# Kernel optimization log

Measured on AMD Instinct MI355X. Metric: run time of the kernel, lower is better.

## Reference

```python
import jax, jax.numpy as jnp
import numpy as np

N_QUBITS = 12
N_LAYERS = 3


def _apply_1q(state, U, q):
    # state: (2,)*N_QUBITS complex64, U: (2,2) single-qubit gate on wire q
    r = jnp.tensordot(U, state, axes=([1], [q]))
    return jnp.moveaxis(r, 0, q)


def _apply_cnot(state, c, t):
    M = jnp.array([[1, 0, 0, 0], [0, 1, 0, 0], [0, 0, 0, 1], [0, 0, 1, 0]],
                  jnp.complex64).reshape(2, 2, 2, 2)
    r = jnp.tensordot(M, state, axes=([2, 3], [c, t]))
    return jnp.moveaxis(r, (0, 1), (c, t))


def circuit_expvals(weights):
    # weights: (N_LAYERS, N_QUBITS, 3). Circuit starts from |0...0> (the
    # TorchLayer 'inputs' arg is a dummy and unused in the original qnode).
    state = jnp.zeros((2,) * N_QUBITS, jnp.complex64).at[(0,) * N_QUBITS].set(1.0)
    zero = jnp.zeros((), jnp.complex64)
    for l in range(N_LAYERS):
        for q in range(N_QUBITS):
            tx, ty, tz = weights[l, q, 0], weights[l, q, 1], weights[l, q, 2]
            cx = jnp.cos(tx / 2).astype(jnp.complex64)
            sx = jnp.sin(tx / 2).astype(jnp.complex64)
            RX = jnp.stack([jnp.stack([cx, -1j * sx]), jnp.stack([-1j * sx, cx])])
            cy = jnp.cos(ty / 2).astype(jnp.complex64)
            sy = jnp.sin(ty / 2).astype(jnp.complex64)
            RY = jnp.stack([jnp.stack([cy, -sy]), jnp.stack([sy, cy])])
            tzc = tz.astype(jnp.complex64)
            em, ep = jnp.exp(-1j * tzc / 2), jnp.exp(1j * tzc / 2)
            RZ = jnp.stack([jnp.stack([em, zero]), jnp.stack([zero, ep])])
            # RX then RY then RZ applied to the state => matrix RZ @ RY @ RX
            state = _apply_1q(state, RZ @ RY @ RX, q)
        for q in range(N_QUBITS):
            state = _apply_cnot(state, q, (q + 1) % N_QUBITS)
    probs = state.real ** 2 + state.imag ** 2
    exps = []
    for q in range(N_QUBITS):
        marg = probs.sum(axis=tuple(a for a in range(N_QUBITS) if a != q))  # (2,)
        exps.append(marg[0] - marg[1])  # <Z_q>
    return jnp.stack(exps).astype(jnp.float32)  # (12,)


def setup_inputs() -> dict:
    key = jax.random.key(0)
    ks = jax.random.split(key, 5)
    B = 1048576
    images = jax.random.uniform(ks[0], (B, 1, 4, 4), dtype=jnp.float32)
    qweights = jax.random.normal(ks[1], (N_LAYERS, N_QUBITS, 3), dtype=jnp.float32)
    W1 = jax.random.normal(ks[2], (32, 12), dtype=jnp.float32) * (1.0 / np.sqrt(12))
    b1 = jnp.zeros((32,), jnp.float32)
    W2 = jax.random.normal(ks[3], (16, 32), dtype=jnp.float32) * (1.0 / np.sqrt(32))
    b2 = jnp.zeros((16,), jnp.float32)
    return {"images": images, "qweights": qweights, "W1": W1, "b1": b1,
            "W2": W2, "b2": b2}


def reference(images, qweights, W1, b1, W2, b2):
    # The original forward ignores the amplitude-encoded image state and runs
    # the identical circuit (dummy zero input) for every batch element, so the
    # per-sample result is constant across the batch.
    z = circuit_expvals(qweights)                     # (12,)
    h = jax.nn.relu(z @ W1.T + b1)                    # (32,)
    pix = jax.nn.sigmoid(h @ W2.T + b2)               # (16,)
    B = images.shape[0]
    return jnp.broadcast_to(pix.reshape(1, 1, 4, 4), (B, 1, 4, 4))
```

## Files before the change

kernel.cpp:

```cpp
#include <hip/hip_runtime.h>
#include <math.h>

#define NQ  12
#define NST 4096

__device__ __forceinline__ int P(int i) { return i ^ ((i >> 4) & 0xF); }

__device__ __forceinline__ void apply2(const float4& u0, const float4& u1,
                                       float2& v0, float2& v1) {
    const float n0r = u0.x*v0.x - u0.y*v0.y + u0.z*v1.x - u0.w*v1.y;
    const float n0i = u0.x*v0.y + u0.y*v0.x + u0.z*v1.y + u0.w*v1.x;
    const float n1r = u1.x*v0.x - u1.y*v0.y + u1.z*v1.x - u1.w*v1.y;
    const float n1i = u1.x*v0.y + u1.y*v0.x + u1.z*v1.y + u1.w*v1.x;
    v0 = make_float2(n0r, n0i);
    v1 = make_float2(n1r, n1i);
}

__global__ __launch_bounds__(1024) void circuit_kernel(
    const float* __restrict__ qw,
    const float* __restrict__ W1,
    const float* __restrict__ b1,
    const float* __restrict__ W2,
    const float* __restrict__ b2,
    float* __restrict__ pix)
{
    __shared__ float2 amp[NST];
    __shared__ float2 cs[108];
    __shared__ float4 gmat[36][2];
    __shared__ float  szv[NQ];
    __shared__ float  sh[32];

    const int tid = threadIdx.x;

    for (int i = tid; i < NST; i += 1024) amp[i] = make_float2(0.f, 0.f);
    if (tid == 0) amp[0] = make_float2(1.f, 0.f);
    if (tid < 108) {
        const float a = 0.5f * qw[tid];
        cs[tid] = make_float2(cosf(a), sinf(a));
    }
    __syncthreads();
    if (tid < 36) {
        const float cx = cs[3*tid+0].x, sx = cs[3*tid+0].y;
        const float cy = cs[3*tid+1].x, sy = cs[3*tid+1].y;
        const float cz = cs[3*tid+2].x, sz = cs[3*tid+2].y;
        const float a00r =  cy*cx, a00i =  sy*sx;
        const float a01r = -sy*cx, a01i = -cy*sx;
        const float a10r =  sy*cx, a10i = -cy*sx;
        const float a11r =  cy*cx, a11i = -sy*sx;
        gmat[tid][0] = make_float4(cz*a00r + sz*a00i, cz*a00i - sz*a00r,
                                   cz*a01r + sz*a01i, cz*a01i - sz*a01r);
        gmat[tid][1] = make_float4(cz*a10r - sz*a10i, cz*a10i + sz*a10r,
                                   cz*a11r - sz*a11i, cz*a11i + sz*a11r);
    }
    __syncthreads();

    for (int l = 0; l < 3; ++l) {
        for (int j = 0; j < 6; ++j) {
            const int g = l*12 + 2*j;
            const float4 ua0 = gmat[g][0],   ua1 = gmat[g][1];
            const float4 ub0 = gmat[g+1][0], ub1 = gmat[g+1][1];
            const int pb = 10 - 2*j;
            const int bb = 1 << pb, ba = bb << 1;
            const int base = ((tid >> pb) << (pb + 2)) | (tid & (bb - 1));
            const int i00 = P(base),      i01 = P(base | bb);
            const int i10 = P(base | ba), i11 = P(base | ba | bb);
            float2 v00 = amp[i00], v01 = amp[i01];
            float2 v10 = amp[i10], v11 = amp[i11];
            apply2(ua0, ua1, v00, v10);
            apply2(ua0, ua1, v01, v11);
            apply2(ub0, ub1, v00, v01);
            apply2(ub0, ub1, v10, v11);
            amp[i00] = v00; amp[i01] = v01; amp[i10] = v10; amp[i11] = v11;
            __syncthreads();
        }
        {
            int dst[4]; float2 val[4];
            #pragma unroll
            for (int k = 0; k < 4; ++k) {
                const int f = tid + 1024*k;
                val[k] = amp[P(f)];
                int t = f;
                t ^= t >> 1; t ^= t >> 2; t ^= t >> 4; t ^= t >> 8;
                const int gd = (t & 0x7FF) | (((t ^ (f >> 11)) & 1) << 11);
                dst[k] = P(gd);
            }
            __syncthreads();
            #pragma unroll
            for (int k = 0; k < 4; ++k) amp[dst[k]] = val[k];
            __syncthreads();
        }
    }

    const int lane = tid & 63;
    const int w    = tid >> 6;
    if (w < NQ) {
        const int bit = 1 << (11 - w);
        float s = 0.f;
        for (int i = lane; i < NST; i += 64) {
            const float2 a = amp[P(i)];
            const float pr = a.x*a.x + a.y*a.y;
            s += (i & bit) ? -pr : pr;
        }
        #pragma unroll
        for (int off = 32; off > 0; off >>= 1) s += __shfl_down(s, off, 64);
        if (lane == 0) szv[w] = s;
    }
    __syncthreads();

    if (tid < 32) {
        float acc = b1[tid];
        #pragma unroll
        for (int k = 0; k < 12; ++k) acc += W1[tid*12 + k] * szv[k];
        sh[tid] = acc > 0.f ? acc : 0.f;
    }
    __syncthreads();
    if (tid < 16) {
        float acc = b2[tid];
        #pragma unroll
        for (int k = 0; k < 32; ++k) acc += W2[tid*32 + k] * sh[k];
        pix[tid] = 1.f / (1.f + expf(-acc));
    }
}

__global__ __launch_bounds__(256) void bcast_kernel(
    const float4* __restrict__ pix4, float4* __restrict__ out4)
{
    const int i = blockIdx.x * 256 + threadIdx.x;
    out4[i] = pix4[i & 3];
}

extern "C" void kernel_launch(void* const* d_in, const int* in_sizes, int n_in,
                              void* d_out, int out_size, void* d_ws, size_t ws_size,
                              hipStream_t stream) {
    const float* qw = (const float*)d_in[1];
    const float* W1 = (const float*)d_in[2];
    const float* b1 = (const float*)d_in[3];
    const float* W2 = (const float*)d_in[4];
    const float* b2 = (const float*)d_in[5];
    float* pix = (float*)d_ws;

    circuit_kernel<<<1, 1024, 0, stream>>>(qw, W1, b1, W2, b2, pix);

    const int n4 = out_size / 4;
    bcast_kernel<<<n4 / 256, 256, 0, stream>>>((const float4*)pix,
                                               (float4*)d_out);
}
```

Baseline: 133.4 us.

## Restructure circuit simulation with product-state first layer and 3-qubit register passes

Rewrites the single-block circuit kernel. The first layer is built analytically as a product state, since it acts on |0…0>. The remaining two layers apply three qubits' gates per pass on 8 amplitudes held in registers, with a new swizzle, which cuts the number of barriers and LDS round trips. The CNOT permutation is folded into the store of the last pass of each layer, and the Z expectation values are accumulated in registers during the final pass and then reduced with shuffles. The block size drops to 512 threads. The total runtime is likely dominated by the broadcast kernel writing 16M floats, so the gain is probably small.

```diff
diff --git a/kernel.cpp b/kernel.cpp
--- a/kernel.cpp
+++ b/kernel.cpp
@@ -1,12 +1,20 @@
 #include <hip/hip_runtime.h>
 #include <math.h>
 
-#define NQ  12
-#define NST 4096
-
-__device__ __forceinline__ int P(int i) { return i ^ ((i >> 4) & 0xF); }
-
-__device__ __forceinline__ void apply2(const float4& u0, const float4& u1,
+#define NTH 512
+
+__device__ __forceinline__ int Sw(int i) { return i ^ ((i >> 6) & 7); }
+
+__device__ __forceinline__ int Fr(int i) {
+    int x = i; x ^= x >> 1; x ^= x >> 2; x ^= x >> 4; x ^= x >> 8;
+    return (x & 0x7FF) | (((x ^ (i >> 11)) & 1) << 11);
+}
+
+__device__ __forceinline__ float2 cmul(float2 a, float2 b) {
+    return make_float2(a.x*b.x - a.y*b.y, a.x*b.y + a.y*b.x);
+}
+
+__device__ __forceinline__ void apply2(const float4 u0, const float4 u1,
                                        float2& v0, float2& v1) {
     const float n0r = u0.x*v0.x - u0.y*v0.y + u0.z*v1.x - u0.w*v1.y;
     const float n0i = u0.x*v0.y + u0.y*v0.x + u0.z*v1.y + u0.w*v1.x;
@@ -16,7 +24,51 @@
     v1 = make_float2(n1r, n1i);
 }
 
-__global__ __launch_bounds__(1024) void circuit_kernel(
+template<int PLOW, int MODE>
+__device__ __forceinline__ void do_pass(float2* amp, const float4 (*gmat)[2],
+                                        int gbase, int t, float* zacc) {
+    int base;
+    if      (PLOW == 9) base = t;
+    else if (PLOW == 6) base = ((t >> 6) << 9) | (t & 63);
+    else if (PLOW == 3) base = ((t >> 3) << 6) | (t & 7);
+    else                base = t << 3;
+
+    float2 v[8]; int idx[8];
+    #pragma unroll
+    for (int r = 0; r < 8; ++r) {
+        idx[r] = Sw(base | (r << PLOW));
+        v[r] = amp[idx[r]];
+    }
+    #pragma unroll
+    for (int k = 2; k >= 0; --k) {
+        const int q = 11 - (PLOW + k);
+        const float4 u0 = gmat[gbase + q][0];
+        const float4 u1 = gmat[gbase + q][1];
+        const int m = 1 << k;
+        #pragma unroll
+        for (int r = 0; r < 8; ++r)
+            if (!(r & m)) apply2(u0, u1, v[r], v[r | m]);
+    }
+    if (MODE == 0) {
+        #pragma unroll
+        for (int r = 0; r < 8; ++r) amp[idx[r]] = v[r];
+    } else if (MODE == 1) {
+        __syncthreads();
+        #pragma unroll
+        for (int r = 0; r < 8; ++r) amp[Sw(Fr(base | (r << PLOW)))] = v[r];
+    } else {
+        #pragma unroll
+        for (int r = 0; r < 8; ++r) {
+            const int x = Fr(base | (r << PLOW));
+            const float p = v[r].x*v[r].x + v[r].y*v[r].y;
+            #pragma unroll
+            for (int q = 0; q < 12; ++q)
+                zacc[q] += ((x >> (11 - q)) & 1) ? -p : p;
+        }
+    }
+}
+
+__global__ __launch_bounds__(NTH) void circuit_kernel(
     const float* __restrict__ qw,
     const float* __restrict__ W1,
     const float* __restrict__ b1,
@@ -24,25 +76,19 @@
     const float* __restrict__ b2,
     float* __restrict__ pix)
 {
-    __shared__ float2 amp[NST];
-    __shared__ float2 cs[108];
+    __shared__ float2 amp[4096];
     __shared__ float4 gmat[36][2];
-    __shared__ float  szv[NQ];
+    __shared__ float  zp2[96];
+    __shared__ float  szv[12];
     __shared__ float  sh[32];
 
     const int tid = threadIdx.x;
 
-    for (int i = tid; i < NST; i += 1024) amp[i] = make_float2(0.f, 0.f);
-    if (tid == 0) amp[0] = make_float2(1.f, 0.f);
-    if (tid < 108) {
-        const float a = 0.5f * qw[tid];
-        cs[tid] = make_float2(cosf(a), sinf(a));
-    }
-    __syncthreads();
     if (tid < 36) {
-        const float cx = cs[3*tid+0].x, sx = cs[3*tid+0].y;
-        const float cy = cs[3*tid+1].x, sy = cs[3*tid+1].y;
-        const float cz = cs[3*tid+2].x, sz = cs[3*tid+2].y;
+        float sx, cx, sy, cy, sz, cz;
+        sincosf(0.5f * qw[tid*3+0], &sx, &cx);
+        sincosf(0.5f * qw[tid*3+1], &sy, &cy);
+        sincosf(0.5f * qw[tid*3+2], &sz, &cz);
         const float a00r =  cy*cx, a00i =  sy*sx;
         const float a01r = -sy*cx, a01i = -cy*sx;
         const float a10r =  sy*cx, a10i = -cy*sx;
@@ -54,56 +100,75 @@
     }
     __syncthreads();
 
-    for (int l = 0; l < 3; ++l) {
-        for (int j = 0; j < 6; ++j) {
-            const int g = l*12 + 2*j;
-            const float4 ua0 = gmat[g][0],   ua1 = gmat[g][1];
-            const float4 ub0 = gmat[g+1][0], ub1 = gmat[g+1][1];
-            const int pb = 10 - 2*j;
-            const int bb = 1 << pb, ba = bb << 1;
-            const int base = ((tid >> pb) << (pb + 2)) | (tid & (bb - 1));
-            const int i00 = P(base),      i01 = P(base | bb);
-            const int i10 = P(base | ba), i11 = P(base | ba | bb);
-            float2 v00 = amp[i00], v01 = amp[i01];
-            float2 v10 = amp[i10], v11 = amp[i11];
-            apply2(ua0, ua1, v00, v10);
-            apply2(ua0, ua1, v01, v11);
-            apply2(ub0, ub1, v00, v01);
-            apply2(ub0, ub1, v10, v11);
-            amp[i00] = v00; amp[i01] = v01; amp[i10] = v10; amp[i11] = v11;
-            __syncthreads();
-        }
-        {
-            int dst[4]; float2 val[4];
-            #pragma unroll
-            for (int k = 0; k < 4; ++k) {
-                const int f = tid + 1024*k;
-                val[k] = amp[P(f)];
-                int t = f;
-                t ^= t >> 1; t ^= t >> 2; t ^= t >> 4; t ^= t >> 8;
-                const int gd = (t & 0x7FF) | (((t ^ (f >> 11)) & 1) << 11);
-                dst[k] = P(gd);
-            }
-            __syncthreads();
-            #pragma unroll
-            for (int k = 0; k < 4; ++k) amp[dst[k]] = val[k];
-            __syncthreads();
-        }
-    }
+    {
+        float2 pp = make_float2(1.f, 0.f);
+        #pragma unroll
+        for (int b = 11; b >= 3; --b) {
+            const int q = 11 - b;
+            const float4 g = gmat[q][(tid >> (b - 3)) & 1];
+            pp = cmul(pp, make_float2(g.x, g.y));
+        }
+        float2 c9[2], c10[2], c11[2];
+        #pragma unroll
+        for (int s = 0; s < 2; ++s) {
+            c9[s]  = make_float2(gmat[9][s].x,  gmat[9][s].y);
+            c10[s] = make_float2(gmat[10][s].x, gmat[10][s].y);
+            c11[s] = make_float2(gmat[11][s].x, gmat[11][s].y);
+        }
+        #pragma unroll
+        for (int r = 0; r < 8; ++r) {
+            const float2 v = cmul(pp,
+                cmul(c9[(r>>2)&1], cmul(c10[(r>>1)&1], c11[r&1])));
+            amp[Sw(Fr((tid << 3) | r))] = v;
+        }
+    }
+    __syncthreads();
+
+    float zacc[12];
+    #pragma unroll
+    for (int q = 0; q < 12; ++q) zacc[q] = 0.f;
+
+    do_pass<9,0>(amp, gmat, 12, tid, zacc); __syncthreads();
+    do_pass<6,0>(amp, gmat, 12, tid, zacc); __syncthreads();
+    do_pass<3,0>(amp, gmat, 12, tid, zacc); __syncthreads();
+    do_pass<0,1>(amp, gmat, 12, tid, zacc); __syncthreads();
+    do_pass<9,0>(amp, gmat, 24, tid, zacc); __syncthreads();
+    do_pass<6,0>(amp, gmat, 24, tid, zacc); __syncthreads();
+    do_pass<3,0>(amp, gmat, 24, tid, zacc); __syncthreads();
+    do_pass<0,2>(amp, gmat, 24, tid, zacc);
 
     const int lane = tid & 63;
-    const int w    = tid >> 6;
-    if (w < NQ) {
-        const int bit = 1 << (11 - w);
+    float z6[6];
+    #pragma unroll
+    for (int k = 0; k < 6; ++k) {
+        const float send = (lane & 1) ? zacc[k]     : zacc[k+6];
+        const float keep = (lane & 1) ? zacc[k+6]   : zacc[k];
+        z6[k] = keep + __shfl_xor(send, 1);
+    }
+    float z3[3];
+    #pragma unroll
+    for (int k = 0; k < 3; ++k) {
+        const float send = (lane & 2) ? z6[k]   : z6[k+3];
+        const float keep = (lane & 2) ? z6[k+3] : z6[k];
+        z3[k] = keep + __shfl_xor(send, 2);
+    }
+    #pragma unroll
+    for (int m = 4; m <= 32; m <<= 1) {
+        #pragma unroll
+        for (int k = 0; k < 3; ++k) z3[k] += __shfl_xor(z3[k], m);
+    }
+    if (lane < 4) {
+        const int qb = 6*(lane & 1) + 3*((lane >> 1) & 1);
+        const int w  = tid >> 6;
+        #pragma unroll
+        for (int k = 0; k < 3; ++k) zp2[w*12 + qb + k] = z3[k];
+    }
+    __syncthreads();
+    if (tid < 12) {
         float s = 0.f;
-        for (int i = lane; i < NST; i += 64) {
-            const float2 a = amp[P(i)];
-            const float pr = a.x*a.x + a.y*a.y;
-            s += (i & bit) ? -pr : pr;
-        }
-        #pragma unroll
-        for (int off = 32; off > 0; off >>= 1) s += __shfl_down(s, off, 64);
-        if (lane == 0) szv[w] = s;
+        #pragma unroll
+        for (int w = 0; w < 8; ++w) s += zp2[w*12 + tid];
+        szv[tid] = s;
     }
     __syncthreads();
 
@@ -139,7 +204,7 @@
     const float* b2 = (const float*)d_in[5];
     float* pix = (float*)d_ws;
 
-    circuit_kernel<<<1, 1024, 0, stream>>>(qw, W1, b1, W2, b2, pix);
+    circuit_kernel<<<1, NTH, 0, stream>>>(qw, W1, b1, W2, b2, pix);
 
     const int n4 = out_size / 4;
     bcast_kernel<<<n4 / 256, 256, 0, stream>>>((const float4*)pix,
```

After: 123.3 us. 1.08x faster.
